# Optimization experiments

Measured on AMD Instinct MI355X. Metric: run time of the kernel, lower is better.

## Reference

```python
import jax, jax.numpy as jnp
import numpy as np

EPS = 1e-5

def ln(x, gamma, beta):
    m = jnp.mean(x, axis=-1, keepdims=True)
    std = jnp.sqrt(jnp.var(x, axis=-1, keepdims=True) + EPS)
    return gamma * ((x - m) / (std + EPS)) + beta

def hard_sigmoid(x):
    return jnp.clip(0.2 * x + 0.5, 0.0, 1.0)

def setup_inputs() -> dict:
    key = jax.random.key(0)
    B, T, D, U, UEP = 64, 2048, 256, 256, 64
    ks = jax.random.split(key, 16)
    def gn(k, shape, s=0.05):
        return (jax.random.normal(k, shape, dtype=jnp.float32) * s)
    inp = {}
    inp['x'] = jax.random.normal(ks[0], (B, T, D), dtype=jnp.float32)
    inp['mask'] = jax.random.randint(ks[1], (B, T), 0, 2, dtype=jnp.int32)
    inp['W'] = gn(ks[2], (D, 3 * U))
    inp['U'] = gn(ks[3], (U, 3 * U))
    inp['b'] = jnp.zeros((3 * U,), jnp.float32)
    inp['gammas'] = 1.0 + gn(ks[4], (2, 3 * U), 0.1)
    inp['betas'] = gn(ks[5], (2, 3 * U), 0.1)
    inp['W_EP'] = gn(ks[6], (D, 3 * UEP))
    inp['U_EP'] = gn(ks[7], (UEP, 3 * UEP))
    inp['b_EP'] = jnp.zeros((3 * UEP,), jnp.float32)
    inp['gammas_EP'] = 1.0 + gn(ks[8], (2, 3 * UEP), 0.1)
    inp['betas_EP'] = gn(ks[9], (2, 3 * UEP), 0.1)
    inp['W1_EP'] = gn(ks[10], (UEP, 1))
    inp['b1_EP'] = jnp.zeros((1,), jnp.float32)
    return inp

def _gru_step(s1, h_tm1, Umat, g1, bt1, dim):
    # s1: precomputed ln(x@W + b)  [B, 3*dim]
    s2 = ln(h_tm1 @ Umat[:, :2 * dim], g1[:2 * dim], bt1[:2 * dim])
    s = hard_sigmoid(s1[:, :2 * dim] + s2)
    z, r = s[:, :dim], s[:, dim:2 * dim]
    hh = ln((r * h_tm1) @ Umat[:, 2 * dim:], g1[2 * dim:], bt1[2 * dim:])
    return z * h_tm1 + (1.0 - z) * jnp.tanh(s1[:, 2 * dim:] + hh)

def _encoder(x, mask, W, U, b, gammas, betas, W_EP, U_EP, b_EP, gammas_EP, betas_EP, W1_EP, b1_EP):
    B, T, D = x.shape
    dim = U.shape[0]
    dim_ep = U_EP.shape[0]
    # input projections + their LayerNorms depend only on x -> precompute (same math)
    s1_all = ln(jnp.einsum('btd,dk->btk', x, W) + b, gammas[0], betas[0])          # [B,T,3U]
    s1_ep_all = ln(jnp.einsum('btd,dk->btk', x, W_EP) + b_EP, gammas_EP[0], betas_EP[0])  # [B,T,3Uep]
    s1_all = jnp.swapaxes(s1_all, 0, 1)        # [T,B,3U]
    s1_ep_all = jnp.swapaxes(s1_ep_all, 0, 1)  # [T,B,3Uep]
    xm_all = (mask > 0).T                      # [T,B] bool

    def step(carry, inp):
        h_tm1, hep_tm1, is_end_tm1 = carry
        s1, s1e, xm = inp
        h_tm1 = jnp.where(is_end_tm1[:, None] > 0.5, 0.0, h_tm1)
        h = _gru_step(s1, h_tm1, U, gammas[1], betas[1], dim)
        h = jnp.where(xm[:, None], h, h_tm1)
        hep = _gru_step(s1e, hep_tm1, U_EP, gammas_EP[1], betas_EP[1], dim_ep)
        hep = jnp.where(xm[:, None], hep, hep_tm1)
        is_end = jnp.round(jax.nn.sigmoid(hep_tm1 @ W1_EP + b1_EP))[:, 0]
        return (h, hep, is_end), (h, is_end)

    init = (jnp.zeros((B, dim), x.dtype), jnp.zeros((B, dim_ep), x.dtype), jnp.zeros((B,), x.dtype))
    _, (h_seq, end_seq) = jax.lax.scan(step, init, (s1_all, s1_ep_all, xm_all))
    return jnp.swapaxes(h_seq, 0, 1), jnp.swapaxes(end_seq, 0, 1)  # [B,T,U], [B,T]

def reference(x, mask, W, U, b, gammas, betas, W_EP, U_EP, b_EP, gammas_EP, betas_EP, W1_EP, b1_EP):
    return _encoder(x, mask, W, U, b, gammas, betas, W_EP, U_EP, b_EP, gammas_EP, betas_EP, W1_EP, b1_EP)
```

## Files before the change

### kernel.cpp

```cpp
#include <hip/hip_runtime.h>


typedef _Float16 h2  __attribute__((ext_vector_type(2)));
typedef _Float16 v8h __attribute__((ext_vector_type(8)));

__device__ __forceinline__ float fdot2_(h2 a, h2 b, float c) {
#if __has_builtin(__builtin_amdgcn_fdot2)
  return __builtin_amdgcn_fdot2(a, b, c, false);
#else
  return c + (float)a[0] * (float)b[0] + (float)a[1] * (float)b[1];
#endif
}

template <int I>
__device__ __forceinline__ h2 pr(v8h v) {
  h2 r; r[0] = v[2 * I]; r[1] = v[2 * I + 1]; return r;
}

__device__ __forceinline__ void wg_barrier() {
  __builtin_amdgcn_sched_barrier(0);
  asm volatile("s_waitcnt lgkmcnt(0)" ::: "memory");
  __builtin_amdgcn_sched_barrier(0);
  __builtin_amdgcn_s_barrier();
  __builtin_amdgcn_sched_barrier(0);
}

__global__ __launch_bounds__(256) void prep_kernel(
    const float* __restrict__ W, const float* __restrict__ U,
    const float* __restrict__ W_EP,
    _Float16* __restrict__ wt, _Float16* __restrict__ uzr,
    _Float16* __restrict__ uh, float* __restrict__ wept)
{
  const int blk = blockIdx.x;
  const int k = threadIdx.x;
  if (blk < 768) {
    const int j = blk;
    wt[(size_t)j * 256 + k] = (_Float16)W[(size_t)k * 768 + j];
  } else if (blk < 1280) {
    const int j = blk - 768;
    uzr[(size_t)j * 256 + k] = (_Float16)U[(size_t)k * 768 + j];
  } else if (blk < 1536) {
    const int j = blk - 1280;
    const int p = k >> 3, e = k & 7;
    uh[((size_t)p * 256 + j) * 8 + e] = (_Float16)U[(size_t)k * 768 + 512 + j];
  } else {
    const int j = blk - 1536;
    wept[(size_t)j * 256 + k] = W_EP[(size_t)k * 192 + j];
  }
}

__global__ __launch_bounds__(256) void ph1_main_kernel(
    const float* __restrict__ x, const _Float16* __restrict__ wt,
    const float* __restrict__ bvec, const float* __restrict__ gam,
    const float* __restrict__ bet, _Float16* __restrict__ s1out)
{
  __shared__ __align__(16) _Float16 xs[16][256];
  __shared__ float sp[16][768];
  const int tid = threadIdx.x;
  const size_t row0 = (size_t)blockIdx.x * 16;

  #pragma unroll
  for (int i = 0; i < 16; ++i)
    xs[i][tid] = (_Float16)x[(row0 + i) * 256 + tid];
  __syncthreads();

  #pragma unroll 1
  for (int cc = 0; cc < 3; ++cc) {
    const int col = cc * 256 + tid;
    const v8h* wp = (const v8h*)(wt + (size_t)col * 256);
    float acc[16];
    #pragma unroll
    for (int r = 0; r < 16; ++r) acc[r] = 0.f;
    #pragma unroll 4
    for (int c = 0; c < 32; ++c) {
      const v8h w8 = wp[c];
      #pragma unroll
      for (int r = 0; r < 16; ++r) {
        const v8h x8 = *(const v8h*)(&xs[r][c * 8]);
        acc[r] = fdot2_(pr<0>(x8), pr<0>(w8), acc[r]);
        acc[r] = fdot2_(pr<1>(x8), pr<1>(w8), acc[r]);
        acc[r] = fdot2_(pr<2>(x8), pr<2>(w8), acc[r]);
        acc[r] = fdot2_(pr<3>(x8), pr<3>(w8), acc[r]);
      }
    }
    const float bb = bvec[col];
    #pragma unroll
    for (int r = 0; r < 16; ++r) sp[r][col] = acc[r] + bb;
  }
  __syncthreads();

  const int w = tid >> 6, lane = tid & 63;
  for (int rr = 0; rr < 4; ++rr) {
    const int r = (w << 2) | rr;
    float vals[12], sum = 0.f, sq = 0.f;
    #pragma unroll
    for (int j = 0; j < 12; ++j) {
      const float v = sp[r][lane + (j << 6)];
      vals[j] = v; sum += v; sq += v * v;
    }
    #pragma unroll
    for (int m = 32; m >= 1; m >>= 1) {
      sum += __shfl_xor(sum, m); sq += __shfl_xor(sq, m);
    }
    const float mean = sum * (1.f / 768.f);
    const float var = sq * (1.f / 768.f) - mean * mean;
    const float inv = 1.f / (sqrtf(var + 1e-5f) + 1e-5f);
    #pragma unroll
    for (int j = 0; j < 12; ++j) {
      const int c = lane + (j << 6);
      s1out[(row0 + r) * 768 + c] =
          (_Float16)(gam[c] * ((vals[j] - mean) * inv) + bet[c]);
    }
  }
}

__global__ __launch_bounds__(192) void ph1_ep_kernel(
    const float* __restrict__ x, const float* __restrict__ wept,
    const float* __restrict__ bvec, const float* __restrict__ gam,
    const float* __restrict__ bet, void* __restrict__ s1e, const int store64)
{
  __shared__ __align__(16) float xs[16][256];
  __shared__ double sp[16][192];
  const int tid = threadIdx.x;
  const size_t row0 = (size_t)blockIdx.x * 16;

  for (int idx = tid; idx < 4096; idx += 192)
    xs[idx >> 8][idx & 255] = x[row0 * 256 + idx];
  __syncthreads();

  {
    const float4* wp = (const float4*)(wept + (size_t)tid * 256);
    double acc[16];
    #pragma unroll
    for (int r = 0; r < 16; ++r) acc[r] = 0.0;
    #pragma unroll 2
    for (int c = 0; c < 64; ++c) {
      const float4 w4 = wp[c];
      #pragma unroll
      for (int r = 0; r < 16; ++r) {
        const float4 x4 = *(const float4*)(&xs[r][c * 4]);
        acc[r] += (double)x4.x * (double)w4.x;
        acc[r] += (double)x4.y * (double)w4.y;
        acc[r] += (double)x4.z * (double)w4.z;
        acc[r] += (double)x4.w * (double)w4.w;
      }
    }
    const double bb = (double)bvec[tid];
    #pragma unroll
    for (int r = 0; r < 16; ++r) sp[r][tid] = acc[r] + bb;
  }
  __syncthreads();

  const int w = tid >> 6, lane = tid & 63;
  for (int r = w; r < 16; r += 3) {
    double vals[3], sum = 0.0, sq = 0.0;
    #pragma unroll
    for (int j = 0; j < 3; ++j) {
      const double v = sp[r][lane + (j << 6)];
      vals[j] = v; sum += v; sq += v * v;
    }
    #pragma unroll
    for (int m = 32; m >= 1; m >>= 1) {
      sum += __shfl_xor(sum, m); sq += __shfl_xor(sq, m);
    }
    const double mean = sum * (1.0 / 192.0);
    const double var = sq * (1.0 / 192.0) - mean * mean;
    const double den = sqrt(var + 1e-5) + 1e-5;
    #pragma unroll
    for (int j = 0; j < 3; ++j) {
      const int c = lane + (j << 6);
      const double vv = (double)gam[c] * ((vals[j] - mean) / den) + (double)bet[c];
      if (store64) ((double*)s1e)[(row0 + r) * 192 + c] = vv;
      else         ((float*)s1e)[(row0 + r) * 192 + c] = (float)vv;
    }
  }
}

#define OFF_UH     0
#define OFF_MASK   131072
#define OFF_HEP    139264
#define OFF_ZEE    139776
#define OFF_RHEP   140288
#define OFF_EPZRP  140800
#define OFF_EPHHP  140928
#define OFF_H2     140992
#define OFF_RH     141504
#define OFF_HF     142016
#define OFF_Z      143040
#define OFF_ZRP    144064
#define OFF_HHP    144128
#define OFF_FLAG   144160
#define SCAN_LDS_BYTES 144192

__global__ __launch_bounds__(512, 2) void scan_kernel(
    const _Float16* __restrict__ uzr_g, const _Float16* __restrict__ uh_g,
    const float* __restrict__ U_EP, const _Float16* __restrict__ s1,
    const void* __restrict__ s1e_v, const int s1e64,
    const int* __restrict__ mask,
    const float* __restrict__ gam1, const float* __restrict__ bet1,
    const float* __restrict__ gamep1, const float* __restrict__ betep1,
    const float* __restrict__ W1, const float* __restrict__ b1,
    float* __restrict__ out)
{
  extern __shared__ char sm[];
  const int t = threadIdx.x;
  const int b = blockIdx.x;
  const int w = t >> 6;
  const int je  = t >> 2;
  const int qe  = t & 3;
  const int jeh = (t & 255) >> 2;

  float*  hf    = (float*)(sm + OFF_HF);
  float*  flagp = (float*)(sm + OFF_FLAG);
  double* hepd  = (double*)(sm + OFF_HEP);
  int*    maskl = (int*)(sm + OFF_MASK);

  {
    const v8h* src = (const v8h*)uh_g;
    v8h* dst = (v8h*)(sm + OFF_UH);
    #pragma unroll
    for (int i = 0; i < 16; ++i) dst[i * 512 + t] = src[i * 512 + t];
  }
  #pragma unroll
  for (int i = 0; i < 4; ++i) maskl[i * 512 + t] = mask[((size_t)b << 11) + i * 512 + t];

  float uz[128];
  {
    const float4* up = (const float4*)uzr_g + (size_t)t * 32;
    #pragma unroll
    for (int c = 0; c < 32; ++c) {
      const float4 v = up[c];
      uz[4 * c + 0] = v.x; uz[4 * c + 1] = v.y;
      uz[4 * c + 2] = v.z; uz[4 * c + 3] = v.w;
    }
  }
  #pragma unroll
  for (int i = 0; i < 128; ++i) asm volatile("" : "+v"(uz[i]));

  float uez[16], ueh[16];
  #pragma unroll
  for (int i = 0; i < 16; ++i) uez[i] = U_EP[(size_t)(16 * qe + i) * 192 + je];
  #pragma unroll
  for (int i = 0; i < 16; ++i) ueh[i] = U_EP[(size_t)(16 * qe + i) * 192 + 128 + jeh];

  const float gz = gam1[t],                bz = bet1[t];
  const float gh = gam1[512 + (t & 255)],  bh = bet1[512 + (t & 255)];
  const float gse = gamep1[je],            bse = betep1[je];
  const float ghe = gamep1[128 + jeh],     bhe = betep1[128 + jeh];
  const double w1d = (double)W1[t & 63];
  const double b1d = (double)b1[0];
  const double* dptr = (const double*)s1e_v;
  const float*  fptr = (const float*)s1e_v;

  if (t < 128) { h2 z2; z2[0] = (_Float16)0.f; z2[1] = (_Float16)0.f;
                 ((h2*)(sm + OFF_H2))[t] = z2; }
  if (t < 256) hf[t] = 0.f;
  if (t < 64)  hepd[t] = 0.0;
  if (t < 2)   flagp[t] = 0.f;

  const size_t n0 = (size_t)b << 11;
  float  s1zr_c = (float)s1[n0 * 768 + t];
  float  s1h_c  = (float)s1[n0 * 768 + 512 + (t & 255)];
  double s1ezr_c = s1e64 ? dptr[n0 * 192 + je]
                         : (double)fptr[n0 * 192 + je];
  double s1ehh_c = s1e64 ? dptr[n0 * 192 + 128 + jeh]
                         : (double)fptr[n0 * 192 + 128 + jeh];
  __syncthreads();

  for (int tt = 0; tt < 2048; ++tt) {
    const size_t n = ((size_t)b << 11) | (size_t)tt;
    const float fz = (flagp[tt & 1] > 0.5f) ? 0.f : 1.f;

    if (tt > 0 && t < 256) out[(n - 1) * 256 + t] = hf[t];

    const int ttn = (tt < 2047) ? tt + 1 : 2047;
    const size_t np1 = ((size_t)b << 11) | (size_t)ttn;
    const float  s1zr_n = (float)s1[np1 * 768 + t];
    const float  s1h_n  = (float)s1[np1 * 768 + 512 + (t & 255)];
    const double s1ezr_n = s1e64 ? dptr[np1 * 192 + je]
                                 : (double)fptr[np1 * 192 + je];
    const double s1ehh_n = s1e64 ? dptr[np1 * 192 + 128 + jeh]
                                 : (double)fptr[np1 * 192 + 128 + jeh];

    if (w == 7) {
      double p = hepd[t & 63] * w1d;
      #pragma unroll
      for (int m = 1; m <= 32; m <<= 1) p += __shfl_xor(p, m);
      if (t == 448) {
        const float e = ((p + b1d) > 0.0) ? 1.f : 0.f;
        flagp[(tt + 1) & 1] = e;
        out[(size_t)33554432 + n] = e;
      }
    }

    float d;
    {
      const v8h* hv = (const v8h*)(sm + OFF_H2);
      float a0 = 0.f, a1 = 0.f, a2 = 0.f, a3 = 0.f;
      #pragma unroll
      for (int c = 0; c < 32; ++c) {
        const v8h hc = hv[c];
        a0 = fdot2_(pr<0>(hc), __builtin_bit_cast(h2, uz[4 * c + 0]), a0);
        a1 = fdot2_(pr<1>(hc), __builtin_bit_cast(h2, uz[4 * c + 1]), a1);
        a2 = fdot2_(pr<2>(hc), __builtin_bit_cast(h2, uz[4 * c + 2]), a2);
        a3 = fdot2_(pr<3>(hc), __builtin_bit_cast(h2, uz[4 * c + 3]), a3);
      }
      d = ((a0 + a1) + (a2 + a3)) * fz;
      float s_ = d, q_ = d * d;
      #pragma unroll
      for (int m = 1; m <= 32; m <<= 1) { s_ += __shfl_xor(s_, m); q_ += __shfl_xor(q_, m); }
      if ((t & 63) == 0) ((float2*)(sm + OFF_ZRP))[w] = make_float2(s_, q_);
    }
    double de;
    {
      const double2* hp = (const double2*)(hepd + 16 * qe);
      double acc = 0.0;
      #pragma unroll
      for (int i = 0; i < 8; ++i) {
        const double2 hv2 = hp[i];
        acc += hv2.x * (double)uez[2 * i] + hv2.y * (double)uez[2 * i + 1];
      }
      acc += __shfl_xor(acc, 1); acc += __shfl_xor(acc, 2);
      de = acc;
      double es = de, eq = de * de;
      #pragma unroll
      for (int m = 4; m <= 32; m <<= 1) { es += __shfl_xor(es, m); eq += __shfl_xor(eq, m); }
      if ((t & 63) == 0) ((double2*)(sm + OFF_EPZRP))[w] = make_double2(es, eq);
    }
    wg_barrier();

    {
      float S = 0.f, Q = 0.f;
      const float4* zp = (const float4*)(sm + OFF_ZRP);
      #pragma unroll
      for (int i = 0; i < 4; ++i) { const float4 v = zp[i]; S += v.x + v.z; Q += v.y + v.w; }
      const float mean = S * (1.f / 512.f);
      const float var = Q * (1.f / 512.f) - mean * mean;
      const float inv = 1.f / (sqrtf(var + 1e-5f) + 1e-5f);
      const float s2v = gz * ((d - mean) * inv) + bz;
      float sv = 0.2f * (s1zr_c + s2v) + 0.5f;
      sv = fminf(fmaxf(sv, 0.f), 1.f);
      if (t < 256) ((float*)(sm + OFF_Z))[t] = sv;
      else {
        const float rhv = sv * (fz * hf[t - 256]);
        ((_Float16*)(sm + OFF_RH))[t - 256] = (_Float16)rhv;
      }
    }
    if ((t & 3) == 0) {
      double S = 0.0, Q = 0.0;
      const double2* ep = (const double2*)(sm + OFF_EPZRP);
      #pragma unroll
      for (int i = 0; i < 8; ++i) { S += ep[i].x; Q += ep[i].y; }
      const double mean = S * (1.0 / 128.0);
      const double var = Q * (1.0 / 128.0) - mean * mean;
      const double den = sqrt(var + 1e-5) + 1e-5;
      const double s2e = (double)gse * ((de - mean) / den) + (double)bse;
      double se = 0.2 * (s1ezr_c + s2e) + 0.5;
      se = fmin(fmax(se, 0.0), 1.0);
      if (je < 64) ((double*)(sm + OFF_ZEE))[je] = se;
      else         ((double*)(sm + OFF_RHEP))[je - 64] = se * hepd[je - 64];
    }
    wg_barrier();

    float dh = 0.f;
    double deh = 0.0;
    if (t < 256) {
      const v8h* rhv8 = (const v8h*)(sm + OFF_RH);
      const v8h* uhv  = (const v8h*)(sm + OFF_UH);
      float c0 = 0.f, c1 = 0.f, c2 = 0.f, c3 = 0.f;
      #pragma unroll
      for (int p = 0; p < 32; ++p) {
        const v8h rc = rhv8[p];
        const v8h uc = uhv[p * 256 + t];
        c0 = fdot2_(pr<0>(rc), pr<0>(uc), c0);
        c1 = fdot2_(pr<1>(rc), pr<1>(uc), c1);
        c2 = fdot2_(pr<2>(rc), pr<2>(uc), c2);
        c3 = fdot2_(pr<3>(rc), pr<3>(uc), c3);
      }
      dh = (c0 + c1) + (c2 + c3);
      float s_ = dh, q_ = dh * dh;
      #pragma unroll
      for (int m = 1; m <= 32; m <<= 1) { s_ += __shfl_xor(s_, m); q_ += __shfl_xor(q_, m); }
      if ((t & 63) == 0) ((float2*)(sm + OFF_HHP))[w] = make_float2(s_, q_);
    } else {
      const double2* rp = (const double2*)((double*)(sm + OFF_RHEP) + 16 * qe);
      double acc = 0.0;
      #pragma unroll
      for (int i = 0; i < 8; ++i) {
        const double2 rv = rp[i];
        acc += rv.x * (double)ueh[2 * i] + rv.y * (double)ueh[2 * i + 1];
      }
      acc += __shfl_xor(acc, 1); acc += __shfl_xor(acc, 2);
      deh = acc;
      double es = deh, eq = deh * deh;
      #pragma unroll
      for (int m = 4; m <= 32; m <<= 1) { es += __shfl_xor(es, m); eq += __shfl_xor(eq, m); }
      if ((t & 63) == 0) ((double2*)(sm + OFF_EPHHP))[w - 4] = make_double2(es, eq);
    }
    wg_barrier();

    const int xm = maskl[tt];
    if (t < 256) {
      float S = 0.f, Q = 0.f;
      const float4* hp4 = (const float4*)(sm + OFF_HHP);
      #pragma unroll
      for (int i = 0; i < 2; ++i) { const float4 v = hp4[i]; S += v.x + v.z; Q += v.y + v.w; }
      const float mean = S * (1.f / 256.f);
      const float var = Q * (1.f / 256.f) - mean * mean;
      const float inv = 1.f / (sqrtf(var + 1e-5f) + 1e-5f);
      const float hhv = gh * ((dh - mean) * inv) + bh;
      const float z = ((float*)(sm + OFF_Z))[t];
      const float hzf = fz * hf[t];
      const float hn = z * hzf + (1.f - z) * tanhf(s1h_c + hhv);
      const float hc_ = (xm > 0) ? hn : hzf;
      hf[t] = hc_;
      const float ho = __shfl_xor(hc_, 1);
      if (!(t & 1)) {
        h2 p2; p2[0] = (_Float16)hc_; p2[1] = (_Float16)ho;
        ((h2*)(sm + OFF_H2))[t >> 1] = p2;
      }
    } else if ((t & 3) == 0) {
      double S = 0.0, Q = 0.0;
      const double2* ep = (const double2*)(sm + OFF_EPHHP);
      #pragma unroll
      for (int i = 0; i < 4; ++i) { S += ep[i].x; Q += ep[i].y; }
      const double mean = S * (1.0 / 64.0);
      const double var = Q * (1.0 / 64.0) - mean * mean;
      const double den = sqrt(var + 1e-5) + 1e-5;
      const double hhe = (double)ghe * ((deh - mean) / den) + (double)bhe;
      const double ze = ((double*)(sm + OFF_ZEE))[jeh];
      const double hold = hepd[jeh];
      const double hepn = ze * hold + (1.0 - ze) * tanh(s1ehh_c + hhe);
      hepd[jeh] = (xm > 0) ? hepn : hold;
    }
    wg_barrier();

    s1zr_c = s1zr_n; s1h_c = s1h_n; s1ezr_c = s1ezr_n; s1ehh_c = s1ehh_n;
  }
  if (t < 256) out[((((size_t)b << 11) | 2047)) * 256 + t] = hf[t];
}

extern "C" void kernel_launch(void* const* d_in, const int* in_sizes, int n_in,
                              void* d_out, int out_size, void* d_ws, size_t ws_size,
                              hipStream_t stream)
{
  (void)in_sizes; (void)n_in; (void)out_size;
  const float* x       = (const float*)d_in[0];
  const int*   mask    = (const int*)d_in[1];
  const float* W       = (const float*)d_in[2];
  const float* U       = (const float*)d_in[3];
  const float* bvec    = (const float*)d_in[4];
  const float* gammas  = (const float*)d_in[5];
  const float* betas   = (const float*)d_in[6];
  const float* W_EP    = (const float*)d_in[7];
  const float* U_EP    = (const float*)d_in[8];
  const float* b_EP    = (const float*)d_in[9];
  const float* gammasE = (const float*)d_in[10];
  const float* betasE  = (const float*)d_in[11];
  const float* W1_EP   = (const float*)d_in[12];
  const float* b1_EP   = (const float*)d_in[13];
  float* out = (float*)d_out;

  const size_t NR = 131072;
  const size_t S1_SZ    = NR * 768 * 2;
  const size_t S1E64_SZ = NR * 192 * 8;
  const size_t S1E32_SZ = NR * 192 * 4;
  const size_t WSMALL = 262144 + 131072 + 393216 + 196608;
  const int s1e64 = (ws_size >= S1_SZ + S1E64_SZ + WSMALL) ? 1 : 0;
  const size_t S1E_SZ = s1e64 ? S1E64_SZ : S1E32_SZ;
  if (ws_size < S1_SZ + S1E32_SZ + WSMALL) return;

  char* ws = (char*)d_ws;
  size_t off = 0;
  void* s1e      = (void*)(ws + off);      off += S1E_SZ;
  _Float16* s1   = (_Float16*)(ws + off);  off += S1_SZ;
  _Float16* uzr  = (_Float16*)(ws + off);  off += 262144;
  _Float16* uh   = (_Float16*)(ws + off);  off += 131072;
  _Float16* wt   = (_Float16*)(ws + off);  off += 393216;
  float* wept    = (float*)(ws + off);     off += 196608;

  prep_kernel<<<dim3(1728), dim3(256), 0, stream>>>(
      W, U, W_EP, wt, uzr, uh, wept);
  ph1_main_kernel<<<dim3(8192), dim3(256), 0, stream>>>(
      x, wt, bvec, gammas, betas, s1);
  ph1_ep_kernel<<<dim3(8192), dim3(192), 0, stream>>>(
      x, wept, b_EP, gammasE, betasE, s1e, s1e64);

  hipFuncSetAttribute(reinterpret_cast<const void*>(scan_kernel),
                      hipFuncAttributeMaxDynamicSharedMemorySize, SCAN_LDS_BYTES);
  scan_kernel<<<dim3(64), dim3(512), SCAN_LDS_BYTES, stream>>>(
      uzr, uh, U_EP, s1, (const void*)s1e, s1e64, mask,
      gammas + 768, betas + 768, gammasE + 192, betasE + 192,
      W1_EP, b1_EP, out);
}
```

Baseline: 16.69 ms.

## Split scan into separate EP scan and batched main GRU scan

Moves the end-prediction GRU recurrence into its own kernel, one block of 128 threads per batch row, which writes per-step reset flags to workspace. The main GRU scan then runs four batch rows per 512-thread block (16 blocks), streaming U_zr from global/L2 in a chunked layout instead of keeping it in registers. Each loaded weight chunk is reused across four rows. The aim is to take the EP work off the main critical path and amortize weight loads. The trade-offs are far fewer active CUs, more barriers per step, and weight traffic through the cache on every timestep.

```diff
diff --git a/kernel.cpp b/kernel.cpp
--- a/kernel.cpp
+++ b/kernel.cpp
@@ -15,14 +15,6 @@
 template <int I>
 __device__ __forceinline__ h2 pr(v8h v) {
   h2 r; r[0] = v[2 * I]; r[1] = v[2 * I + 1]; return r;
-}
-
-__device__ __forceinline__ void wg_barrier() {
-  __builtin_amdgcn_sched_barrier(0);
-  asm volatile("s_waitcnt lgkmcnt(0)" ::: "memory");
-  __builtin_amdgcn_sched_barrier(0);
-  __builtin_amdgcn_s_barrier();
-  __builtin_amdgcn_sched_barrier(0);
 }
 
 __global__ __launch_bounds__(256) void prep_kernel(
@@ -38,7 +30,8 @@
     wt[(size_t)j * 256 + k] = (_Float16)W[(size_t)k * 768 + j];
   } else if (blk < 1280) {
     const int j = blk - 768;
-    uzr[(size_t)j * 256 + k] = (_Float16)U[(size_t)k * 768 + j];
+    const int c = k >> 3, e = k & 7;
+    uzr[((size_t)c * 512 + j) * 8 + e] = (_Float16)U[(size_t)k * 768 + j];
   } else if (blk < 1536) {
     const int j = blk - 1280;
     const int p = k >> 3, e = k & 7;
@@ -176,268 +169,339 @@
   }
 }
 
-#define OFF_UH     0
-#define OFF_MASK   131072
-#define OFF_HEP    139264
-#define OFF_ZEE    139776
-#define OFF_RHEP   140288
-#define OFF_EPZRP  140800
-#define OFF_EPHHP  140928
-#define OFF_H2     140992
-#define OFF_RH     141504
-#define OFF_HF     142016
-#define OFF_Z      143040
-#define OFF_ZRP    144064
-#define OFF_HHP    144128
-#define OFF_FLAG   144160
-#define SCAN_LDS_BYTES 144192
-
-__global__ __launch_bounds__(512, 2) void scan_kernel(
-    const _Float16* __restrict__ uzr_g, const _Float16* __restrict__ uh_g,
-    const float* __restrict__ U_EP, const _Float16* __restrict__ s1,
-    const void* __restrict__ s1e_v, const int s1e64,
-    const int* __restrict__ mask,
-    const float* __restrict__ gam1, const float* __restrict__ bet1,
+__global__ __launch_bounds__(128) void ep_scan_kernel(
+    const float* __restrict__ U_EP, const void* __restrict__ s1e_v,
+    const int s1e64, const int* __restrict__ mask,
     const float* __restrict__ gamep1, const float* __restrict__ betep1,
     const float* __restrict__ W1, const float* __restrict__ b1,
+    float* __restrict__ out, float* __restrict__ fzw)
+{
+  __shared__ double hep[64];
+  __shared__ double zeL[64];
+  __shared__ double rhepL[64];
+  __shared__ double prt[4];
+
+  const int t = threadIdx.x;
+  const int b = blockIdx.x;
+  const int lane = t & 63;
+  const int w = t >> 6;
+
+  float uez[64];
+  #pragma unroll
+  for (int k = 0; k < 64; ++k) uez[k] = U_EP[(size_t)k * 192 + t];
+  float uehh[64];
+  if (t < 64) {
+    #pragma unroll
+    for (int k = 0; k < 64; ++k) uehh[k] = U_EP[(size_t)k * 192 + 128 + t];
+  }
+
+  const float gse = gamep1[t],        bse = betep1[t];
+  const float ghe = (t < 64) ? gamep1[128 + t] : 0.f;
+  const float bhe = (t < 64) ? betep1[128 + t] : 0.f;
+  const double w1d = (t >= 64) ? (double)W1[t - 64] : 0.0;
+  const double b1d = (double)b1[0];
+  const double* dptr = (const double*)s1e_v;
+  const float*  fptr = (const float*)s1e_v;
+
+  if (t < 64) hep[t] = 0.0;
+  if (t == 0) fzw[(size_t)b * 2048] = 0.f;
+
+  const size_t n0 = (size_t)b << 11;
+  double s1ez_c = s1e64 ? dptr[n0 * 192 + t] : (double)fptr[n0 * 192 + t];
+  double s1eh_c = 0.0;
+  if (t < 64) s1eh_c = s1e64 ? dptr[n0 * 192 + 128 + t]
+                             : (double)fptr[n0 * 192 + 128 + t];
+  int mask_c = mask[n0];
+  __syncthreads();
+
+  for (int tt = 0; tt < 2048; ++tt) {
+    const size_t n = ((size_t)b << 11) | (size_t)tt;
+    const int ttn = (tt < 2047) ? tt + 1 : 2047;
+    const size_t np1 = ((size_t)b << 11) | (size_t)ttn;
+    const double s1ez_n = s1e64 ? dptr[np1 * 192 + t] : (double)fptr[np1 * 192 + t];
+    double s1eh_n = 0.0;
+    if (t < 64) s1eh_n = s1e64 ? dptr[np1 * 192 + 128 + t]
+                               : (double)fptr[np1 * 192 + 128 + t];
+    const int mask_n = mask[np1];
+
+    double d = 0.0;
+    {
+      const double2* hp = (const double2*)hep;
+      #pragma unroll
+      for (int k2 = 0; k2 < 32; ++k2) {
+        const double2 h2v = hp[k2];
+        d += h2v.x * (double)uez[2 * k2] + h2v.y * (double)uez[2 * k2 + 1];
+      }
+      double es = d, eq = d * d;
+      #pragma unroll
+      for (int m = 1; m <= 32; m <<= 1) { es += __shfl_xor(es, m); eq += __shfl_xor(eq, m); }
+      if (lane == 0) { prt[w * 2] = es; prt[w * 2 + 1] = eq; }
+    }
+    if (w == 1) {
+      double p = hep[lane] * w1d;
+      #pragma unroll
+      for (int m = 1; m <= 32; m <<= 1) p += __shfl_xor(p, m);
+      if (t == 64) {
+        const float e = ((p + b1d) > 0.0) ? 1.f : 0.f;
+        if (tt < 2047) fzw[(size_t)b * 2048 + tt + 1] = e;
+        out[(size_t)33554432 + n] = e;
+      }
+    }
+    __syncthreads();
+
+    {
+      const double S = prt[0] + prt[2];
+      const double Q = prt[1] + prt[3];
+      const double mean = S * (1.0 / 128.0);
+      const double var = Q * (1.0 / 128.0) - mean * mean;
+      const double den = sqrt(var + 1e-5) + 1e-5;
+      const double s2e = (double)gse * ((d - mean) / den) + (double)bse;
+      double se = 0.2 * (s1ez_c + s2e) + 0.5;
+      se = fmin(fmax(se, 0.0), 1.0);
+      if (t < 64) zeL[t] = se;
+      else        rhepL[t - 64] = se * hep[t - 64];
+    }
+    __syncthreads();
+
+    if (t < 64) {
+      const double2* rp = (const double2*)rhepL;
+      double dh = 0.0;
+      #pragma unroll
+      for (int k2 = 0; k2 < 32; ++k2) {
+        const double2 rv = rp[k2];
+        dh += rv.x * (double)uehh[2 * k2] + rv.y * (double)uehh[2 * k2 + 1];
+      }
+      double es = dh, eq = dh * dh;
+      #pragma unroll
+      for (int m = 1; m <= 32; m <<= 1) { es += __shfl_xor(es, m); eq += __shfl_xor(eq, m); }
+      const double mean = es * (1.0 / 64.0);
+      const double var = eq * (1.0 / 64.0) - mean * mean;
+      const double den = sqrt(var + 1e-5) + 1e-5;
+      const double hhe = (double)ghe * ((dh - mean) / den) + (double)bhe;
+      const double ze = zeL[t];
+      const double hold = hep[t];
+      const double hepn = ze * hold + (1.0 - ze) * tanh(s1eh_c + hhe);
+      hep[t] = (mask_c > 0) ? hepn : hold;
+    }
+    __syncthreads();
+
+    s1ez_c = s1ez_n; s1eh_c = s1eh_n; mask_c = mask_n;
+  }
+}
+
+#define OFFB_UH    0
+#define OFFB_H2B   131072
+#define OFFB_RH2B  133120
+#define OFFB_HF    135168
+#define OFFB_ZS    139264
+#define OFFB_ZRP   143360
+#define OFFB_HHP   143616
+#define OFFB_LNZR  143744
+#define OFFB_LNHH  143776
+#define OFFB_FZ    143808
+#define OFFB_MB    143840
+#define SCANB_LDS_BYTES 143872
+
+__global__ __launch_bounds__(512, 1) void main_scan_kernel(
+    const _Float16* __restrict__ uzr_g, const _Float16* __restrict__ uh_g,
+    const _Float16* __restrict__ s1, const int* __restrict__ mask,
+    const float* __restrict__ fzw,
+    const float* __restrict__ gam1, const float* __restrict__ bet1,
     float* __restrict__ out)
 {
   extern __shared__ char sm[];
   const int t = threadIdx.x;
-  const int b = blockIdx.x;
   const int w = t >> 6;
-  const int je  = t >> 2;
-  const int qe  = t & 3;
-  const int jeh = (t & 255) >> 2;
-
-  float*  hf    = (float*)(sm + OFF_HF);
-  float*  flagp = (float*)(sm + OFF_FLAG);
-  double* hepd  = (double*)(sm + OFF_HEP);
-  int*    maskl = (int*)(sm + OFF_MASK);
+  const int b0 = blockIdx.x * 4;
+
+  float* hf   = (float*)(sm + OFFB_HF);
+  float* zs   = (float*)(sm + OFFB_ZS);
+  float* fzl  = (float*)(sm + OFFB_FZ);
+  int*   mbl  = (int*)(sm + OFFB_MB);
 
   {
     const v8h* src = (const v8h*)uh_g;
-    v8h* dst = (v8h*)(sm + OFF_UH);
+    v8h* dst = (v8h*)(sm + OFFB_UH);
     #pragma unroll
     for (int i = 0; i < 16; ++i) dst[i * 512 + t] = src[i * 512 + t];
   }
+
+  const float gz = gam1[t], bz = bet1[t];
+  const float gh = (t < 256) ? gam1[512 + t] : 0.f;
+  const float bh = (t < 256) ? bet1[512 + t] : 0.f;
+
+  if (t < 256) {
+    #pragma unroll
+    for (int r = 0; r < 4; ++r) {
+      hf[r * 256 + t] = 0.f;
+      ((_Float16*)(sm + OFFB_H2B))[r * 256 + t] = (_Float16)0.f;
+    }
+  }
+  if (t < 4)      fzl[t] = fzw[(size_t)(b0 + t) * 2048];
+  else if (t < 8) mbl[t - 4] = mask[(size_t)(b0 + t - 4) << 11];
+
+  float s1z_c[4], s1h_c[4];
   #pragma unroll
-  for (int i = 0; i < 4; ++i) maskl[i * 512 + t] = mask[((size_t)b << 11) + i * 512 + t];
-
-  float uz[128];
-  {
-    const float4* up = (const float4*)uzr_g + (size_t)t * 32;
-    #pragma unroll
-    for (int c = 0; c < 32; ++c) {
-      const float4 v = up[c];
-      uz[4 * c + 0] = v.x; uz[4 * c + 1] = v.y;
-      uz[4 * c + 2] = v.z; uz[4 * c + 3] = v.w;
-    }
-  }
-  #pragma unroll
-  for (int i = 0; i < 128; ++i) asm volatile("" : "+v"(uz[i]));
-
-  float uez[16], ueh[16];
-  #pragma unroll
-  for (int i = 0; i < 16; ++i) uez[i] = U_EP[(size_t)(16 * qe + i) * 192 + je];
-  #pragma unroll
-  for (int i = 0; i < 16; ++i) ueh[i] = U_EP[(size_t)(16 * qe + i) * 192 + 128 + jeh];
-
-  const float gz = gam1[t],                bz = bet1[t];
-  const float gh = gam1[512 + (t & 255)],  bh = bet1[512 + (t & 255)];
-  const float gse = gamep1[je],            bse = betep1[je];
-  const float ghe = gamep1[128 + jeh],     bhe = betep1[128 + jeh];
-  const double w1d = (double)W1[t & 63];
-  const double b1d = (double)b1[0];
-  const double* dptr = (const double*)s1e_v;
-  const float*  fptr = (const float*)s1e_v;
-
-  if (t < 128) { h2 z2; z2[0] = (_Float16)0.f; z2[1] = (_Float16)0.f;
-                 ((h2*)(sm + OFF_H2))[t] = z2; }
-  if (t < 256) hf[t] = 0.f;
-  if (t < 64)  hepd[t] = 0.0;
-  if (t < 2)   flagp[t] = 0.f;
-
-  const size_t n0 = (size_t)b << 11;
-  float  s1zr_c = (float)s1[n0 * 768 + t];
-  float  s1h_c  = (float)s1[n0 * 768 + 512 + (t & 255)];
-  double s1ezr_c = s1e64 ? dptr[n0 * 192 + je]
-                         : (double)fptr[n0 * 192 + je];
-  double s1ehh_c = s1e64 ? dptr[n0 * 192 + 128 + jeh]
-                         : (double)fptr[n0 * 192 + 128 + jeh];
+  for (int r = 0; r < 4; ++r) {
+    const size_t nr = (size_t)(b0 + r) << 11;
+    s1z_c[r] = (float)s1[nr * 768 + t];
+    s1h_c[r] = (t < 256) ? (float)s1[nr * 768 + 512 + t] : 0.f;
+  }
   __syncthreads();
 
   for (int tt = 0; tt < 2048; ++tt) {
-    const size_t n = ((size_t)b << 11) | (size_t)tt;
-    const float fz = (flagp[tt & 1] > 0.5f) ? 0.f : 1.f;
-
-    if (tt > 0 && t < 256) out[(n - 1) * 256 + t] = hf[t];
-
+    float fzr[4]; int xm[4];
+    #pragma unroll
+    for (int r = 0; r < 4; ++r) {
+      fzr[r] = (fzl[(tt & 1) * 4 + r] > 0.5f) ? 0.f : 1.f;
+      xm[r]  = mbl[(tt & 1) * 4 + r];
+    }
+
+    if (tt > 0 && t >= 256) {
+      const int u = t - 256;
+      #pragma unroll
+      for (int r = 0; r < 4; ++r) {
+        const size_t nr = ((size_t)(b0 + r) << 11) | (size_t)(tt - 1);
+        out[nr * 256 + u] = hf[r * 256 + u];
+      }
+    }
     const int ttn = (tt < 2047) ? tt + 1 : 2047;
-    const size_t np1 = ((size_t)b << 11) | (size_t)ttn;
-    const float  s1zr_n = (float)s1[np1 * 768 + t];
-    const float  s1h_n  = (float)s1[np1 * 768 + 512 + (t & 255)];
-    const double s1ezr_n = s1e64 ? dptr[np1 * 192 + je]
-                                 : (double)fptr[np1 * 192 + je];
-    const double s1ehh_n = s1e64 ? dptr[np1 * 192 + 128 + jeh]
-                                 : (double)fptr[np1 * 192 + 128 + jeh];
-
-    if (w == 7) {
-      double p = hepd[t & 63] * w1d;
-      #pragma unroll
-      for (int m = 1; m <= 32; m <<= 1) p += __shfl_xor(p, m);
-      if (t == 448) {
-        const float e = ((p + b1d) > 0.0) ? 1.f : 0.f;
-        flagp[(tt + 1) & 1] = e;
-        out[(size_t)33554432 + n] = e;
-      }
-    }
-
-    float d;
+    float s1z_n[4], s1h_n[4];
+    #pragma unroll
+    for (int r = 0; r < 4; ++r) {
+      const size_t nr = ((size_t)(b0 + r) << 11) | (size_t)ttn;
+      s1z_n[r] = (float)s1[nr * 768 + t];
+      s1h_n[r] = (t < 256) ? (float)s1[nr * 768 + 512 + t] : 0.f;
+    }
+    float fz_pf = 0.f; int mb_pf = 0;
+    if (t < 4)      fz_pf = fzw[(size_t)(b0 + t) * 2048 + ttn];
+    else if (t < 8) mb_pf = mask[((size_t)(b0 + t - 4) << 11) + ttn];
+
+    float acc[4];
+    #pragma unroll
+    for (int r = 0; r < 4; ++r) acc[r] = 0.f;
     {
-      const v8h* hv = (const v8h*)(sm + OFF_H2);
-      float a0 = 0.f, a1 = 0.f, a2 = 0.f, a3 = 0.f;
-      #pragma unroll
+      const v8h* uzb = (const v8h*)uzr_g;
+      const v8h* hb  = (const v8h*)(sm + OFFB_H2B);
+      #pragma unroll 4
       for (int c = 0; c < 32; ++c) {
-        const v8h hc = hv[c];
-        a0 = fdot2_(pr<0>(hc), __builtin_bit_cast(h2, uz[4 * c + 0]), a0);
-        a1 = fdot2_(pr<1>(hc), __builtin_bit_cast(h2, uz[4 * c + 1]), a1);
-        a2 = fdot2_(pr<2>(hc), __builtin_bit_cast(h2, uz[4 * c + 2]), a2);
-        a3 = fdot2_(pr<3>(hc), __builtin_bit_cast(h2, uz[4 * c + 3]), a3);
-      }
-      d = ((a0 + a1) + (a2 + a3)) * fz;
-      float s_ = d, q_ = d * d;
+        const v8h wc = uzb[(size_t)c * 512 + t];
+        #pragma unroll
+        for (int r = 0; r < 4; ++r) {
+          const v8h hc = hb[r * 32 + c];
+          acc[r] = fdot2_(pr<0>(hc), pr<0>(wc), acc[r]);
+          acc[r] = fdot2_(pr<1>(hc), pr<1>(wc), acc[r]);
+          acc[r] = fdot2_(pr<2>(hc), pr<2>(wc), acc[r]);
+          acc[r] = fdot2_(pr<3>(hc), pr<3>(wc), acc[r]);
+        }
+      }
+    }
+    #pragma unroll
+    for (int r = 0; r < 4; ++r) {
+      acc[r] *= fzr[r];
+      float s_ = acc[r], q_ = acc[r] * acc[r];
       #pragma unroll
       for (int m = 1; m <= 32; m <<= 1) { s_ += __shfl_xor(s_, m); q_ += __shfl_xor(q_, m); }
-      if ((t & 63) == 0) ((float2*)(sm + OFF_ZRP))[w] = make_float2(s_, q_);
-    }
-    double de;
-    {
-      const double2* hp = (const double2*)(hepd + 16 * qe);
-      double acc = 0.0;
-      #pragma unroll
-      for (int i = 0; i < 8; ++i) {
-        const double2 hv2 = hp[i];
-        acc += hv2.x * (double)uez[2 * i] + hv2.y * (double)uez[2 * i + 1];
-      }
-      acc += __shfl_xor(acc, 1); acc += __shfl_xor(acc, 2);
-      de = acc;
-      double es = de, eq = de * de;
-      #pragma unroll
-      for (int m = 4; m <= 32; m <<= 1) { es += __shfl_xor(es, m); eq += __shfl_xor(eq, m); }
-      if ((t & 63) == 0) ((double2*)(sm + OFF_EPZRP))[w] = make_double2(es, eq);
-    }
-    wg_barrier();
-
-    {
+      if ((t & 63) == 0) ((float2*)(sm + OFFB_ZRP))[w * 4 + r] = make_float2(s_, q_);
+    }
+    __syncthreads();
+
+    if (t < 4) {
+      const float2* zp = (const float2*)(sm + OFFB_ZRP);
       float S = 0.f, Q = 0.f;
-      const float4* zp = (const float4*)(sm + OFF_ZRP);
-      #pragma unroll
-      for (int i = 0; i < 4; ++i) { const float4 v = zp[i]; S += v.x + v.z; Q += v.y + v.w; }
+      #pragma unroll
+      for (int i = 0; i < 8; ++i) { S += zp[i * 4 + t].x; Q += zp[i * 4 + t].y; }
       const float mean = S * (1.f / 512.f);
       const float var = Q * (1.f / 512.f) - mean * mean;
       const float inv = 1.f / (sqrtf(var + 1e-5f) + 1e-5f);
-      const float s2v = gz * ((d - mean) * inv) + bz;
-      float sv = 0.2f * (s1zr_c + s2v) + 0.5f;
+      ((float2*)(sm + OFFB_LNZR))[t] = make_float2(mean, inv);
+    }
+    __syncthreads();
+
+    #pragma unroll
+    for (int r = 0; r < 4; ++r) {
+      const float2 ln = ((const float2*)(sm + OFFB_LNZR))[r];
+      const float s2v = gz * ((acc[r] - ln.x) * ln.y) + bz;
+      float sv = 0.2f * (s1z_c[r] + s2v) + 0.5f;
       sv = fminf(fmaxf(sv, 0.f), 1.f);
-      if (t < 256) ((float*)(sm + OFF_Z))[t] = sv;
+      if (t < 256) zs[r * 256 + t] = sv;
       else {
-        const float rhv = sv * (fz * hf[t - 256]);
-        ((_Float16*)(sm + OFF_RH))[t - 256] = (_Float16)rhv;
-      }
-    }
-    if ((t & 3) == 0) {
-      double S = 0.0, Q = 0.0;
-      const double2* ep = (const double2*)(sm + OFF_EPZRP);
-      #pragma unroll
-      for (int i = 0; i < 8; ++i) { S += ep[i].x; Q += ep[i].y; }
-      const double mean = S * (1.0 / 128.0);
-      const double var = Q * (1.0 / 128.0) - mean * mean;
-      const double den = sqrt(var + 1e-5) + 1e-5;
-      const double s2e = (double)gse * ((de - mean) / den) + (double)bse;
-      double se = 0.2 * (s1ezr_c + s2e) + 0.5;
-      se = fmin(fmax(se, 0.0), 1.0);
-      if (je < 64) ((double*)(sm + OFF_ZEE))[je] = se;
-      else         ((double*)(sm + OFF_RHEP))[je - 64] = se * hepd[je - 64];
-    }
-    wg_barrier();
-
-    float dh = 0.f;
-    double deh = 0.0;
+        const float rhv = sv * (fzr[r] * hf[r * 256 + (t - 256)]);
+        ((_Float16*)(sm + OFFB_RH2B))[r * 256 + (t - 256)] = (_Float16)rhv;
+      }
+    }
+    __syncthreads();
+
+    float hacc[4];
+    #pragma unroll
+    for (int r = 0; r < 4; ++r) hacc[r] = 0.f;
     if (t < 256) {
-      const v8h* rhv8 = (const v8h*)(sm + OFF_RH);
-      const v8h* uhv  = (const v8h*)(sm + OFF_UH);
-      float c0 = 0.f, c1 = 0.f, c2 = 0.f, c3 = 0.f;
-      #pragma unroll
-      for (int p = 0; p < 32; ++p) {
-        const v8h rc = rhv8[p];
-        const v8h uc = uhv[p * 256 + t];
-        c0 = fdot2_(pr<0>(rc), pr<0>(uc), c0);
-        c1 = fdot2_(pr<1>(rc), pr<1>(uc), c1);
-        c2 = fdot2_(pr<2>(rc), pr<2>(uc), c2);
-        c3 = fdot2_(pr<3>(rc), pr<3>(uc), c3);
-      }
-      dh = (c0 + c1) + (c2 + c3);
-      float s_ = dh, q_ = dh * dh;
-      #pragma unroll
-      for (int m = 1; m <= 32; m <<= 1) { s_ += __shfl_xor(s_, m); q_ += __shfl_xor(q_, m); }
-      if ((t & 63) == 0) ((float2*)(sm + OFF_HHP))[w] = make_float2(s_, q_);
-    } else {
-      const double2* rp = (const double2*)((double*)(sm + OFF_RHEP) + 16 * qe);
-      double acc = 0.0;
-      #pragma unroll
-      for (int i = 0; i < 8; ++i) {
-        const double2 rv = rp[i];
-        acc += rv.x * (double)ueh[2 * i] + rv.y * (double)ueh[2 * i + 1];
-      }
-      acc += __shfl_xor(acc, 1); acc += __shfl_xor(acc, 2);
-      deh = acc;
-      double es = deh, eq = deh * deh;
-      #pragma unroll
-      for (int m = 4; m <= 32; m <<= 1) { es += __shfl_xor(es, m); eq += __shfl_xor(eq, m); }
-      if ((t & 63) == 0) ((double2*)(sm + OFF_EPHHP))[w - 4] = make_double2(es, eq);
-    }
-    wg_barrier();
-
-    const int xm = maskl[tt];
-    if (t < 256) {
+      const v8h* uhv = (const v8h*)(sm + OFFB_UH);
+      const v8h* rb  = (const v8h*)(sm + OFFB_RH2B);
+      #pragma unroll 4
+      for (int c = 0; c < 32; ++c) {
+        const v8h uc = uhv[c * 256 + t];
+        #pragma unroll
+        for (int r = 0; r < 4; ++r) {
+          const v8h rc = rb[r * 32 + c];
+          hacc[r] = fdot2_(pr<0>(rc), pr<0>(uc), hacc[r]);
+          hacc[r] = fdot2_(pr<1>(rc), pr<1>(uc), hacc[r]);
+          hacc[r] = fdot2_(pr<2>(rc), pr<2>(uc), hacc[r]);
+          hacc[r] = fdot2_(pr<3>(rc), pr<3>(uc), hacc[r]);
+        }
+      }
+      #pragma unroll
+      for (int r = 0; r < 4; ++r) {
+        float s_ = hacc[r], q_ = hacc[r] * hacc[r];
+        #pragma unroll
+        for (int m = 1; m <= 32; m <<= 1) { s_ += __shfl_xor(s_, m); q_ += __shfl_xor(q_, m); }
+        if ((t & 63) == 0) ((float2*)(sm + OFFB_HHP))[w * 4 + r] = make_float2(s_, q_);
+      }
+    }
+    __syncthreads();
+
+    if (t < 4) {
+      const float2* hp = (const float2*)(sm + OFFB_HHP);
       float S = 0.f, Q = 0.f;
-      const float4* hp4 = (const float4*)(sm + OFF_HHP);
-      #pragma unroll
-      for (int i = 0; i < 2; ++i) { const float4 v = hp4[i]; S += v.x + v.z; Q += v.y + v.w; }
+      #pragma unroll
+      for (int i = 0; i < 4; ++i) { S += hp[i * 4 + t].x; Q += hp[i * 4 + t].y; }
       const float mean = S * (1.f / 256.f);
       const float var = Q * (1.f / 256.f) - mean * mean;
       const float inv = 1.f / (sqrtf(var + 1e-5f) + 1e-5f);
-      const float hhv = gh * ((dh - mean) * inv) + bh;
-      const float z = ((float*)(sm + OFF_Z))[t];
-      const float hzf = fz * hf[t];
-      const float hn = z * hzf + (1.f - z) * tanhf(s1h_c + hhv);
-      const float hc_ = (xm > 0) ? hn : hzf;
-      hf[t] = hc_;
-      const float ho = __shfl_xor(hc_, 1);
-      if (!(t & 1)) {
-        h2 p2; p2[0] = (_Float16)hc_; p2[1] = (_Float16)ho;
-        ((h2*)(sm + OFF_H2))[t >> 1] = p2;
-      }
-    } else if ((t & 3) == 0) {
-      double S = 0.0, Q = 0.0;
-      const double2* ep = (const double2*)(sm + OFF_EPHHP);
-      #pragma unroll
-      for (int i = 0; i < 4; ++i) { S += ep[i].x; Q += ep[i].y; }
-      const double mean = S * (1.0 / 64.0);
-      const double var = Q * (1.0 / 64.0) - mean * mean;
-      const double den = sqrt(var + 1e-5) + 1e-5;
-      const double hhe = (double)ghe * ((deh - mean) / den) + (double)bhe;
-      const double ze = ((double*)(sm + OFF_ZEE))[jeh];
-      const double hold = hepd[jeh];
-      const double hepn = ze * hold + (1.0 - ze) * tanh(s1ehh_c + hhe);
-      hepd[jeh] = (xm > 0) ? hepn : hold;
-    }
-    wg_barrier();
-
-    s1zr_c = s1zr_n; s1h_c = s1h_n; s1ezr_c = s1ezr_n; s1ehh_c = s1ehh_n;
-  }
-  if (t < 256) out[((((size_t)b << 11) | 2047)) * 256 + t] = hf[t];
+      ((float2*)(sm + OFFB_LNHH))[t] = make_float2(mean, inv);
+    }
+    __syncthreads();
+
+    if (t < 256) {
+      #pragma unroll
+      for (int r = 0; r < 4; ++r) {
+        const float2 ln = ((const float2*)(sm + OFFB_LNHH))[r];
+        const float hhv = gh * ((hacc[r] - ln.x) * ln.y) + bh;
+        const float z = zs[r * 256 + t];
+        const float hz = fzr[r] * hf[r * 256 + t];
+        const float hn = z * hz + (1.f - z) * tanhf(s1h_c[r] + hhv);
+        const float hc = (xm[r] > 0) ? hn : hz;
+        hf[r * 256 + t] = hc;
+        ((_Float16*)(sm + OFFB_H2B))[r * 256 + t] = (_Float16)hc;
+      }
+    } else if (t < 260) {
+      fzl[((tt + 1) & 1) * 4 + (t - 256)] = 0.f;
+    }
+    if (t < 4)      fzl[((tt + 1) & 1) * 4 + t] = fz_pf;
+    else if (t < 8) mbl[((tt + 1) & 1) * 4 + (t - 4)] = mb_pf;
+    __syncthreads();
+
+    #pragma unroll
+    for (int r = 0; r < 4; ++r) { s1z_c[r] = s1z_n[r]; s1h_c[r] = s1h_n[r]; }
+  }
+  if (t >= 256) {
+    const int u = t - 256;
+    #pragma unroll
+    for (int r = 0; r < 4; ++r) {
+      const size_t nr = ((size_t)(b0 + r) << 11) | (size_t)2047;
+      out[nr * 256 + u] = hf[r * 256 + u];
+    }
+  }
 }
 
 extern "C" void kernel_launch(void* const* d_in, const int* in_sizes, int n_in,
@@ -465,7 +529,7 @@
   const size_t S1_SZ    = NR * 768 * 2;
   const size_t S1E64_SZ = NR * 192 * 8;
   const size_t S1E32_SZ = NR * 192 * 4;
-  const size_t WSMALL = 262144 + 131072 + 393216 + 196608;
+  const size_t WSMALL = 262144 + 131072 + 393216 + 196608 + 524288;
   const int s1e64 = (ws_size >= S1_SZ + S1E64_SZ + WSMALL) ? 1 : 0;
   const size_t S1E_SZ = s1e64 ? S1E64_SZ : S1E32_SZ;
   if (ws_size < S1_SZ + S1E32_SZ + WSMALL) return;
@@ -478,6 +542,7 @@
   _Float16* uh   = (_Float16*)(ws + off);  off += 131072;
   _Float16* wt   = (_Float16*)(ws + off);  off += 393216;
   float* wept    = (float*)(ws + off);     off += 196608;
+  float* fzw     = (float*)(ws + off);     off += 524288;
 
   prep_kernel<<<dim3(1728), dim3(256), 0, stream>>>(
       W, U, W_EP, wt, uzr, uh, wept);
@@ -486,10 +551,12 @@
   ph1_ep_kernel<<<dim3(8192), dim3(192), 0, stream>>>(
       x, wept, b_EP, gammasE, betasE, s1e, s1e64);
 
-  hipFuncSetAttribute(reinterpret_cast<const void*>(scan_kernel),
-                      hipFuncAttributeMaxDynamicSharedMemorySize, SCAN_LDS_BYTES);
-  scan_kernel<<<dim3(64), dim3(512), SCAN_LDS_BYTES, stream>>>(
-      uzr, uh, U_EP, s1, (const void*)s1e, s1e64, mask,
-      gammas + 768, betas + 768, gammasE + 192, betasE + 192,
-      W1_EP, b1_EP, out);
-}
+  ep_scan_kernel<<<dim3(64), dim3(128), 0, stream>>>(
+      U_EP, (const void*)s1e, s1e64, mask,
+      gammasE + 192, betasE + 192, W1_EP, b1_EP, out, fzw);
+
+  hipFuncSetAttribute(reinterpret_cast<const void*>(main_scan_kernel),
+                      hipFuncAttributeMaxDynamicSharedMemorySize, SCANB_LDS_BYTES);
+  main_scan_kernel<<<dim3(16), dim3(512), SCANB_LDS_BYTES, stream>>>(
+      uzr, uh, s1, mask, fzw, gammas + 768, betas + 768, out);
+}
```

New measurement: 41.68 ms. 2.5x slower.
